# Kernel tuning notes

Hardware: AMD Instinct MI355X
Metric: run time of the kernel (lower is better)

The kernel has to match this reference:

```python
import jax, jax.numpy as jnp
import numpy as np

B, L, D, DA, NL = 32, 2048, 512, 512, 512

def setup_inputs() -> dict:
    key = jax.random.key(0)
    k1, k2, k3, k4 = jax.random.split(key, 4)
    std = 0.03
    return {
        "x": jax.random.normal(k1, (B, L, D), dtype=jnp.float32),
        "W1": jax.random.normal(k2, (DA, D), dtype=jnp.float32) * std,   # first_linears[0].weight [d_a, size]
        "W2": jax.random.normal(k3, (NL, DA), dtype=jnp.float32) * std,  # second_linears[0].weight [n_labels, d_a]
        "W3": jax.random.normal(k4, (NL, D), dtype=jnp.float32) * std,   # third_linears[0].weight [n_labels, size]
        "b3": jnp.zeros((NL,), dtype=jnp.float32),                        # third_linears[0].bias
    }

def reference(x, W1, W2, W3, b3):
    # weights = tanh(first_linear(x)) : [B, L, DA]
    w = jnp.tanh(jnp.einsum("bld,ad->bla", x, W1))
    # att logits : [B, L, NL]; softmax over seq dim (dim=1), then transpose -> [B, NL, L]
    att = jax.nn.softmax(jnp.einsum("bla,na->bln", w, W2), axis=1)
    att_weights = jnp.swapaxes(att, 1, 2)  # [B, NL, L]
    # context_vector = att_weights @ x : [B, NL, D]
    context_vector = jnp.einsum("bnl,bld->bnd", att_weights, x)
    # label-wise diagonal mul-sum-add: [B, NL]
    weighted_output = jnp.einsum("bnd,nd->bn", context_vector, W3) + b3
    return (context_vector, weighted_output, att_weights)
```

## Files before the change

kernel.cpp:

```cpp
#include <hip/hip_runtime.h>
#include <math.h>

#define BB 32
#define LL 2048
#define DD 512
#define DA_ 512
#define NL_ 512

typedef __bf16 bf16;
typedef __bf16 bf16x8 __attribute__((ext_vector_type(8)));
typedef __bf16 bf16x4 __attribute__((ext_vector_type(4)));
typedef float floatx4 __attribute__((ext_vector_type(4)));

__device__ __forceinline__ void dma16(const void* g, void* l) {
    __builtin_amdgcn_global_load_lds((__attribute__((address_space(1))) void*)g,
                                     (__attribute__((address_space(3))) void*)l,
                                     16, 0, 0);
}

__device__ __forceinline__ float fast_tanh(float x) {
    const float e = __expf(2.f * x);
    return 1.f - 2.f * __builtin_amdgcn_rcpf(e + 1.f);
}

__device__ __forceinline__ void gemm_core(const bf16* __restrict__ A,
                                          const bf16* __restrict__ B,
                                          int K, int lda, int ldb,
                                          floatx4 acc[4][4])
{
    __shared__ bf16 As[128 * 32];
    __shared__ bf16 Bs[128 * 32];
    const int tid = threadIdx.x;
    const int lane = tid & 63, wv = tid >> 6;
    const int wr = wv >> 1, wc = wv & 1;
    const int lm = lane & 15, quad = lane >> 4;

    for (int k0 = 0; k0 < K; k0 += 32) {
        __syncthreads();
        #pragma unroll
        for (int it = 0; it < 2; ++it) {
            const int c = tid + it * 256;
            const int row = c >> 2, kq = c & 3;
            dma16(A + (size_t)row * lda + k0 + kq * 8, As + c * 8);
        }
        #pragma unroll
        for (int it = 0; it < 2; ++it) {
            const int c = tid + it * 256;
            const int row = c >> 2, kq = c & 3;
            dma16(B + (size_t)row * ldb + k0 + kq * 8, Bs + c * 8);
        }
        __syncthreads();

        bf16x8 af[4], bfr[4];
        #pragma unroll
        for (int t = 0; t < 4; ++t) {
            af[t]  = *(const bf16x8*)(As + (wr * 64 + t * 16 + lm) * 32 + quad * 8);
            bfr[t] = *(const bf16x8*)(Bs + (wc * 64 + t * 16 + lm) * 32 + quad * 8);
        }
        #pragma unroll
        for (int i = 0; i < 4; ++i)
            #pragma unroll
            for (int j = 0; j < 4; ++j)
                acc[i][j] = __builtin_amdgcn_mfma_f32_16x16x32_bf16(af[i], bfr[j], acc[i][j], 0, 0, 0);
    }
}

__global__ __launch_bounds__(256) void k_cvt(const float* __restrict__ src,
                                             bf16* __restrict__ dst, int n)
{
    const int i = (blockIdx.x * 256 + threadIdx.x) * 4;
    if (i < n) {
        const float4 v = *(const float4*)(src + i);
        bf16x4 p = {(bf16)v.x, (bf16)v.y, (bf16)v.z, (bf16)v.w};
        *(bf16x4*)(dst + i) = p;
    }
}

__global__ __launch_bounds__(256) void k_transpose(const float* __restrict__ x,
                                                   bf16* __restrict__ xT,
                                                   bf16* __restrict__ xb)
{
    __shared__ float T[64][68];
    const int b = blockIdx.z;
    const int l0 = blockIdx.x * 64, d0 = blockIdx.y * 64;
    const int tid = threadIdx.x;
    const float* xsrc = x + ((size_t)b * LL + l0) * DD + d0;
    bf16* xbdst = xb + ((size_t)b * LL + l0) * DD + d0;
    #pragma unroll
    for (int it = 0; it < 4; ++it) {
        const int c = tid + it * 256;
        const int lr = c >> 4, cc = (c & 15) * 4;
        const float4 v = *(const float4*)(xsrc + (size_t)lr * DD + cc);
        T[lr][cc] = v.x; T[lr][cc + 1] = v.y; T[lr][cc + 2] = v.z; T[lr][cc + 3] = v.w;
        bf16x4 p = {(bf16)v.x, (bf16)v.y, (bf16)v.z, (bf16)v.w};
        *(bf16x4*)(xbdst + (size_t)lr * DD + cc) = p;
    }
    __syncthreads();
    const int dl = tid >> 2, ls = (tid & 3) * 16;
    bf16x8 p0, p1;
    #pragma unroll
    for (int j = 0; j < 8; ++j) p0[j] = (bf16)T[ls + j][dl];
    #pragma unroll
    for (int j = 0; j < 8; ++j) p1[j] = (bf16)T[ls + 8 + j][dl];
    bf16* o = xT + ((size_t)b * DD + d0 + dl) * LL + l0 + ls;
    *(bf16x8*)o = p0;
    *(bf16x8*)(o + 8) = p1;
}

__global__ __launch_bounds__(256) void k_gemm1(const bf16* __restrict__ xb,
                                               const bf16* __restrict__ W1b,
                                               bf16* __restrict__ wb)
{
    const int n0 = blockIdx.x * 128;
    const size_t m0 = (size_t)blockIdx.y * 128;
    floatx4 acc[4][4];
    #pragma unroll
    for (int i = 0; i < 4; ++i)
        #pragma unroll
        for (int j = 0; j < 4; ++j) { floatx4 z = {0.f, 0.f, 0.f, 0.f}; acc[i][j] = z; }
    gemm_core(xb + m0 * DD, W1b + (size_t)n0 * DD, DD, DD, DD, acc);

    const int tid = threadIdx.x, lane = tid & 63, wv = tid >> 6;
    const int wr = wv >> 1, wc = wv & 1, lm = lane & 15, quad = lane >> 4;
    const size_t row0 = m0 + wr * 64 + quad * 4;
    const int col0 = n0 + wc * 64 + lm;
    #pragma unroll
    for (int i = 0; i < 4; ++i)
        #pragma unroll
        for (int j = 0; j < 4; ++j)
            #pragma unroll
            for (int r = 0; r < 4; ++r)
                wb[(row0 + i * 16 + r) * DA_ + col0 + j * 16] = (bf16)fast_tanh(acc[i][j][r]);
}

__global__ __launch_bounds__(256) void k_gemm2(const bf16* __restrict__ wb,
                                               const bf16* __restrict__ W2b,
                                               bf16* __restrict__ logitsb)
{
    const int c0 = blockIdx.x * 128;
    const int m0 = blockIdx.y * 128;
    floatx4 acc[4][4];
    #pragma unroll
    for (int i = 0; i < 4; ++i)
        #pragma unroll
        for (int j = 0; j < 4; ++j) { floatx4 z = {0.f, 0.f, 0.f, 0.f}; acc[i][j] = z; }
    gemm_core(W2b + (size_t)m0 * DA_, wb + (size_t)c0 * DA_, DA_, DA_, DA_, acc);

    const int b = c0 >> 11, lloc = c0 & (LL - 1);
    const int tid = threadIdx.x, lane = tid & 63, wv = tid >> 6;
    const int wr = wv >> 1, wc = wv & 1, lm = lane & 15, quad = lane >> 4;
    bf16* base = logitsb + ((size_t)b * NL_ + m0 + wr * 64 + quad * 4) * LL
               + lloc + wc * 64 + lm;
    #pragma unroll
    for (int i = 0; i < 4; ++i)
        #pragma unroll
        for (int j = 0; j < 4; ++j)
            #pragma unroll
            for (int r = 0; r < 4; ++r)
                base[(size_t)(i * 16 + r) * LL + j * 16] = (bf16)acc[i][j][r];
}

__global__ __launch_bounds__(256) void k_softmax(const bf16* __restrict__ logitsb,
                                                 float* __restrict__ att,
                                                 bf16* __restrict__ attb)
{
    const int tid = threadIdx.x;
    const bf16* p = logitsb + (size_t)blockIdx.x * LL;
    float* po = att + (size_t)blockIdx.x * LL;
    bf16* pb = attb + (size_t)blockIdx.x * LL;

    const bf16x8 v = *(const bf16x8*)(p + tid * 8);
    float f[8];
    #pragma unroll
    for (int j = 0; j < 8; ++j) f[j] = (float)v[j];

    __shared__ float red[8];
    float m = f[0];
    #pragma unroll
    for (int j = 1; j < 8; ++j) m = fmaxf(m, f[j]);
    #pragma unroll
    for (int off = 32; off; off >>= 1) m = fmaxf(m, __shfl_down(m, off));
    if ((tid & 63) == 0) red[tid >> 6] = m;
    __syncthreads();
    m = fmaxf(fmaxf(red[0], red[1]), fmaxf(red[2], red[3]));

    float s = 0.f;
    #pragma unroll
    for (int j = 0; j < 8; ++j) { f[j] = __expf(f[j] - m); s += f[j]; }
    #pragma unroll
    for (int off = 32; off; off >>= 1) s += __shfl_down(s, off);
    if ((tid & 63) == 0) red[4 + (tid >> 6)] = s;
    __syncthreads();
    s = red[4] + red[5] + red[6] + red[7];

    const float inv = 1.0f / s;
    float4 o0, o1;
    o0.x = f[0] * inv; o0.y = f[1] * inv; o0.z = f[2] * inv; o0.w = f[3] * inv;
    o1.x = f[4] * inv; o1.y = f[5] * inv; o1.z = f[6] * inv; o1.w = f[7] * inv;
    *(float4*)(po + tid * 8) = o0;
    *(float4*)(po + tid * 8 + 4) = o1;
    bf16x8 q = {(bf16)o0.x, (bf16)o0.y, (bf16)o0.z, (bf16)o0.w,
                (bf16)o1.x, (bf16)o1.y, (bf16)o1.z, (bf16)o1.w};
    *(bf16x8*)(pb + tid * 8) = q;
}

__global__ __launch_bounds__(256) void k_gemm3(const bf16* __restrict__ attb,
                                               const bf16* __restrict__ xT,
                                               float* __restrict__ ctx)
{
    const int b = blockIdx.z;
    const int n0 = blockIdx.x * 128;
    const int m0 = blockIdx.y * 128;
    floatx4 acc[4][4];
    #pragma unroll
    for (int i = 0; i < 4; ++i)
        #pragma unroll
        for (int j = 0; j < 4; ++j) { floatx4 z = {0.f, 0.f, 0.f, 0.f}; acc[i][j] = z; }
    gemm_core(attb + ((size_t)b * NL_ + m0) * LL,
              xT + ((size_t)b * DD + n0) * LL, LL, LL, LL, acc);

    const int tid = threadIdx.x, lane = tid & 63, wv = tid >> 6;
    const int wr = wv >> 1, wc = wv & 1, lm = lane & 15, quad = lane >> 4;
    float* base = ctx + ((size_t)b * NL_ + m0 + wr * 64 + quad * 4) * DD
                + n0 + wc * 64 + lm;
    #pragma unroll
    for (int i = 0; i < 4; ++i)
        #pragma unroll
        for (int j = 0; j < 4; ++j)
            #pragma unroll
            for (int r = 0; r < 4; ++r)
                base[(size_t)(i * 16 + r) * DD + j * 16] = acc[i][j][r];
}

__global__ __launch_bounds__(256) void k_wo(
    const float* __restrict__ ctx, const float* __restrict__ W3,
    const float* __restrict__ b3, float* __restrict__ wo)
{
    const int gw = blockIdx.x * 4 + (threadIdx.x >> 6);
    const int lane = threadIdx.x & 63;
    const int n = gw & (NL_ - 1);
    const float* c = ctx + (size_t)gw * DD;
    const float* w = W3 + (size_t)n * DD;
    float s = 0.f;
    #pragma unroll
    for (int it = 0; it < 2; ++it) {
        const float4 a = *(const float4*)&c[(it * 64 + lane) * 4];
        const float4 b = *(const float4*)&w[(it * 64 + lane) * 4];
        s += a.x * b.x + a.y * b.y + a.z * b.z + a.w * b.w;
    }
    #pragma unroll
    for (int off = 32; off; off >>= 1) s += __shfl_down(s, off);
    if (lane == 0) wo[gw] = s + b3[n];
}

extern "C" void kernel_launch(void* const* d_in, const int* in_sizes, int n_in,
                              void* d_out, int out_size, void* d_ws, size_t ws_size,
                              hipStream_t stream)
{
    const float* x  = (const float*)d_in[0];
    const float* W1 = (const float*)d_in[1];
    const float* W2 = (const float*)d_in[2];
    const float* W3 = (const float*)d_in[3];
    const float* b3 = (const float*)d_in[4];

    float* out = (float*)d_out;
    float* ctx = out;
    float* wo  = out + (size_t)BB * NL_ * DD;
    float* att = wo + (size_t)BB * NL_;

    char* wsp = (char*)d_ws;
    const size_t M64 = (size_t)64 * 1024 * 1024;
    bf16* xT      = (bf16*)(wsp);
    bf16* xb      = (bf16*)(wsp + M64);
    bf16* logitsb = (bf16*)(wsp + M64);
    bf16* wb      = (bf16*)(wsp + 2 * M64);
    bf16* attb    = (bf16*)(wsp + 2 * M64);
    bf16* W1b     = (bf16*)(wsp + 3 * M64);
    bf16* W2b     = W1b + (size_t)DA_ * DD;

    k_cvt<<<(DA_ * DD) / 1024, 256, 0, stream>>>(W1, W1b, DA_ * DD);
    k_cvt<<<(NL_ * DA_) / 1024, 256, 0, stream>>>(W2, W2b, NL_ * DA_);
    k_transpose<<<dim3(LL / 64, DD / 64, BB), 256, 0, stream>>>(x, xT, xb);
    k_gemm1<<<dim3(DA_ / 128, (BB * LL) / 128), 256, 0, stream>>>(xb, W1b, wb);
    k_gemm2<<<dim3((BB * LL) / 128, NL_ / 128), 256, 0, stream>>>(wb, W2b, logitsb);
    k_softmax<<<BB * NL_, 256, 0, stream>>>(logitsb, att, attb);
    k_gemm3<<<dim3(DD / 128, NL_ / 128, BB), 256, 0, stream>>>(attb, xT, ctx);
    k_wo<<<(BB * NL_) / 4, 256, 0, stream>>>(ctx, W3, b3, wo);
}
```

Measured before the change: 525.2 us.

## Double-buffer GEMM LDS loads and fuse label-wise dot product into gemm3 epilogue

The shared GEMM core now uses two LDS buffers, so the next K-tile is fetched by global_load_lds while MFMAs run on the current one, and the MFMA block is bracketed with s_setprio. This replaces two barriers per iteration with one and is meant to hide load latency. Separately, the k_wo kernel is removed: gemm3 computes partial dot products with W3 in its epilogue and atomically adds them into wo, which a new small kernel pre-initializes with b3. The fusion avoids re-reading ctx, but float atomics make the summation order nondeterministic and double buffering doubles LDS use, which may lower occupancy.

Result: no change. 522.7 us (-0.5%).

```diff
diff --git a/kernel.cpp b/kernel.cpp
--- a/kernel.cpp
+++ b/kernel.cpp
@@ -28,40 +28,47 @@
                                           int K, int lda, int ldb,
                                           floatx4 acc[4][4])
 {
-    __shared__ bf16 As[128 * 32];
-    __shared__ bf16 Bs[128 * 32];
+    __shared__ bf16 As[2][128 * 32];
+    __shared__ bf16 Bs[2][128 * 32];
     const int tid = threadIdx.x;
     const int lane = tid & 63, wv = tid >> 6;
     const int wr = wv >> 1, wc = wv & 1;
     const int lm = lane & 15, quad = lane >> 4;
 
-    for (int k0 = 0; k0 < K; k0 += 32) {
-        __syncthreads();
-        #pragma unroll
-        for (int it = 0; it < 2; ++it) {
-            const int c = tid + it * 256;
-            const int row = c >> 2, kq = c & 3;
-            dma16(A + (size_t)row * lda + k0 + kq * 8, As + c * 8);
+    const bf16* a0 = A + (size_t)(tid >> 2) * lda + (tid & 3) * 8;
+    const bf16* b0 = B + (size_t)(tid >> 2) * ldb + (tid & 3) * 8;
+    const size_t a1 = (size_t)64 * lda, b1 = (size_t)64 * ldb;
+
+    dma16(a0,      &As[0][tid * 8]);
+    dma16(a0 + a1, &As[0][2048 + tid * 8]);
+    dma16(b0,      &Bs[0][tid * 8]);
+    dma16(b0 + b1, &Bs[0][2048 + tid * 8]);
+    __syncthreads();
+
+    const int nk = K >> 5;
+    for (int t = 0; t < nk; ++t) {
+        const int cur = t & 1;
+        if (t + 1 < nk) {
+            const int k0 = (t + 1) << 5;
+            dma16(a0 + k0,      &As[cur ^ 1][tid * 8]);
+            dma16(a0 + a1 + k0, &As[cur ^ 1][2048 + tid * 8]);
+            dma16(b0 + k0,      &Bs[cur ^ 1][tid * 8]);
+            dma16(b0 + b1 + k0, &Bs[cur ^ 1][2048 + tid * 8]);
         }
-        #pragma unroll
-        for (int it = 0; it < 2; ++it) {
-            const int c = tid + it * 256;
-            const int row = c >> 2, kq = c & 3;
-            dma16(B + (size_t)row * ldb + k0 + kq * 8, Bs + c * 8);
+        bf16x8 af[4], bfr[4];
+        #pragma unroll
+        for (int tt = 0; tt < 4; ++tt) {
+            af[tt]  = *(const bf16x8*)(&As[cur][(wr * 64 + tt * 16 + lm) * 32 + quad * 8]);
+            bfr[tt] = *(const bf16x8*)(&Bs[cur][(wc * 64 + tt * 16 + lm) * 32 + quad * 8]);
         }
-        __syncthreads();
-
-        bf16x8 af[4], bfr[4];
-        #pragma unroll
-        for (int t = 0; t < 4; ++t) {
-            af[t]  = *(const bf16x8*)(As + (wr * 64 + t * 16 + lm) * 32 + quad * 8);
-            bfr[t] = *(const bf16x8*)(Bs + (wc * 64 + t * 16 + lm) * 32 + quad * 8);
-        }
+        __builtin_amdgcn_s_setprio(1);
         #pragma unroll
         for (int i = 0; i < 4; ++i)
             #pragma unroll
             for (int j = 0; j < 4; ++j)
                 acc[i][j] = __builtin_amdgcn_mfma_f32_16x16x32_bf16(af[i], bfr[j], acc[i][j], 0, 0, 0);
+        __builtin_amdgcn_s_setprio(0);
+        __syncthreads();
     }
 }
 
@@ -74,6 +81,13 @@
         bf16x4 p = {(bf16)v.x, (bf16)v.y, (bf16)v.z, (bf16)v.w};
         *(bf16x4*)(dst + i) = p;
     }
+}
+
+__global__ __launch_bounds__(256) void k_init_wo(const float* __restrict__ b3,
+                                                 float* __restrict__ wo)
+{
+    const int i = blockIdx.x * 256 + threadIdx.x;
+    wo[i] = b3[i & (NL_ - 1)];
 }
 
 __global__ __launch_bounds__(256) void k_transpose(const float* __restrict__ x,
@@ -206,7 +220,9 @@
 
 __global__ __launch_bounds__(256) void k_gemm3(const bf16* __restrict__ attb,
                                                const bf16* __restrict__ xT,
-                                               float* __restrict__ ctx)
+                                               float* __restrict__ ctx,
+                                               const float* __restrict__ W3,
+                                               float* __restrict__ wo)
 {
     const int b = blockIdx.z;
     const int n0 = blockIdx.x * 128;
@@ -230,27 +246,23 @@
             #pragma unroll
             for (int r = 0; r < 4; ++r)
                 base[(size_t)(i * 16 + r) * DD + j * 16] = acc[i][j][r];
-}
-
-__global__ __launch_bounds__(256) void k_wo(
-    const float* __restrict__ ctx, const float* __restrict__ W3,
-    const float* __restrict__ b3, float* __restrict__ wo)
-{
-    const int gw = blockIdx.x * 4 + (threadIdx.x >> 6);
-    const int lane = threadIdx.x & 63;
-    const int n = gw & (NL_ - 1);
-    const float* c = ctx + (size_t)gw * DD;
-    const float* w = W3 + (size_t)n * DD;
-    float s = 0.f;
-    #pragma unroll
-    for (int it = 0; it < 2; ++it) {
-        const float4 a = *(const float4*)&c[(it * 64 + lane) * 4];
-        const float4 b = *(const float4*)&w[(it * 64 + lane) * 4];
-        s += a.x * b.x + a.y * b.y + a.z * b.z + a.w * b.w;
+
+    const int nbase = m0 + wr * 64 + quad * 4;
+    const int dbase = n0 + wc * 64 + lm;
+    #pragma unroll
+    for (int i = 0; i < 4; ++i) {
+        #pragma unroll
+        for (int r = 0; r < 4; ++r) {
+            const int n = nbase + i * 16 + r;
+            float s = 0.f;
+            #pragma unroll
+            for (int j = 0; j < 4; ++j)
+                s += acc[i][j][r] * W3[(size_t)n * DD + dbase + j * 16];
+            #pragma unroll
+            for (int off = 8; off; off >>= 1) s += __shfl_down(s, off);
+            if (lm == 0) atomicAdd(&wo[(size_t)b * NL_ + n], s);
+        }
     }
-    #pragma unroll
-    for (int off = 32; off; off >>= 1) s += __shfl_down(s, off);
-    if (lane == 0) wo[gw] = s + b3[n];
 }
 
 extern "C" void kernel_launch(void* const* d_in, const int* in_sizes, int n_in,
@@ -280,10 +292,10 @@
 
     k_cvt<<<(DA_ * DD) / 1024, 256, 0, stream>>>(W1, W1b, DA_ * DD);
     k_cvt<<<(NL_ * DA_) / 1024, 256, 0, stream>>>(W2, W2b, NL_ * DA_);
+    k_init_wo<<<(BB * NL_) / 256, 256, 0, stream>>>(b3, wo);
     k_transpose<<<dim3(LL / 64, DD / 64, BB), 256, 0, stream>>>(x, xT, xb);
     k_gemm1<<<dim3(DA_ / 128, (BB * LL) / 128), 256, 0, stream>>>(xb, W1b, wb);
     k_gemm2<<<dim3((BB * LL) / 128, NL_ / 128), 256, 0, stream>>>(wb, W2b, logitsb);
     k_softmax<<<BB * NL_, 256, 0, stream>>>(logitsb, att, attb);
-    k_gemm3<<<dim3(DD / 128, NL_ / 128, BB), 256, 0, stream>>>(attb, xT, ctx);
-    k_wo<<<(BB * NL_) / 4, 256, 0, stream>>>(ctx, W3, b3, wo);
-}
+    k_gemm3<<<dim3(DD / 128, NL_ / 128, BB), 256, 0, stream>>>(attb, xT, ctx, W3, wo);
+}
```
